# Optimization experiments

Measured on AMD Instinct MI355X. Metric: run time of the kernel, lower is better.

Reference implementation:

```python
import jax, jax.numpy as jnp
import numpy as np

N, F, H, C = 50000, 128, 256, 40
E = 800000
L, J = 3, 2
TOT = 7  # sum_{i<L} J**i


def setup_inputs() -> dict:
    key = jax.random.key(0)
    ks = jax.random.split(key, 16)
    def rn(k, shape, scale):
        return jax.random.normal(k, shape, jnp.float32) * scale
    w = lambda k, shape: rn(k, shape, 1.0 / np.sqrt(shape[0]).astype(np.float32))
    return {
        "x": rn(ks[0], (N, F), 1.0),
        "feature": rn(ks[1], (TOT, N, F), 1.0),
        "src": jax.random.randint(ks[2], (E,), 0, N),
        "dst": jax.random.randint(ks[3], (E,), 0, N),
        "conv_W0": w(ks[4], (F, H)),       "conv_b0": jnp.zeros((H,), jnp.float32),
        "conv_W1": w(ks[5], (2 * H, H)),   "conv_b1": jnp.zeros((H,), jnp.float32),
        "conv_W2": w(ks[6], (2 * H, H)),   "conv_b2": jnp.zeros((H,), jnp.float32),
        "lin_W0": w(ks[7], (F, H)),        "lin_b0": jnp.zeros((H,), jnp.float32),
        "lin_W1": w(ks[8], (2 * F, H)),    "lin_b1": jnp.zeros((H,), jnp.float32),
        "lin_W2": w(ks[9], (4 * F, H)),    "lin_b2": jnp.zeros((H,), jnp.float32),
        "order_weights": rn(ks[10], (J,), 1.0 / np.sqrt(J).astype(np.float32)),
        "cls_W": w(ks[11], (2 * H, C)),    "cls_b": jnp.zeros((C,), jnp.float32),
    }


def reference(x, feature, src, dst,
              conv_W0, conv_b0, conv_W1, conv_b1, conv_W2, conv_b2,
              lin_W0, lin_b0, lin_W1, lin_b1, lin_W2, lin_b2,
              order_weights, cls_W, cls_b):
    # GCN normalization with self-loops (A-hat = D^-1/2 (A+I) D^-1/2)
    loop = jnp.arange(N, dtype=src.dtype)
    src_sl = jnp.concatenate([src, loop])   # [E+N]
    dst_sl = jnp.concatenate([dst, loop])
    deg = jax.ops.segment_sum(jnp.ones_like(dst_sl, jnp.float32), dst_sl, num_segments=N)
    dinv = jax.lax.rsqrt(deg)  # deg >= 1 thanks to self loops
    norm = dinv[src_sl] * dinv[dst_sl]      # [E+N]

    def gcn(h, W, b):
        m = h @ W                            # transform first (smaller gather)
        agg = jax.ops.segment_sum(m[src_sl] * norm[:, None], dst_sl, num_segments=N)
        return agg + b

    conv_W = [conv_W0, conv_W1, conv_W2]
    conv_b = [conv_b0, conv_b1, conv_b2]
    lin_W = [lin_W0, lin_W1, lin_W2]
    lin_b = [lin_b0, lin_b1, lin_b2]

    comb = x
    begin = 0
    for i in range(L):
        convx = jax.nn.relu(gcn(comb, conv_W[i], conv_b[i]))  # [N, H]
        count = J ** i
        lf = feature[begin:begin + count]                      # [count, N, F]
        if i > 0:
            ow = jnp.tile(order_weights, J ** (i - 1)).reshape(-1, 1, 1)
            lf = ow * lf
        lf = jnp.moveaxis(lf, 0, 1).reshape(N, count * F)      # [N, count*F]
        lin_sct = jax.nn.relu(lf @ lin_W[i] + lin_b[i])        # [N, H]
        comb = jnp.concatenate([lin_sct, convx], axis=-1)      # [N, 2H]
        begin += count
    logits = gcn(comb, cls_W, cls_b)                           # [N, C]
    return jax.nn.log_softmax(logits, axis=-1), logits
```

## Files before the change

### kernel.cpp

```cpp
#include <hip/hip_runtime.h>

#define DEVI __device__ __forceinline__

namespace {

constexpr int Nn = 50000;
constexpr int Ne = 800000;
constexpr int Fd = 128;
constexpr int Hd = 256;
constexpr int Cd = 40;
constexpr int NB = (Nn + 255) / 256;

typedef __attribute__((ext_vector_type(8))) short s16x8;
typedef __attribute__((ext_vector_type(8))) unsigned short u16x8;
typedef __attribute__((ext_vector_type(4))) float f32x4;

DEVI unsigned short f2bf(float f) {
  unsigned int u = __builtin_bit_cast(unsigned int, f);
  u += 0x7fffu + ((u >> 16) & 1u);
  return (unsigned short)(u >> 16);
}
DEVI float bf2f(unsigned short s) {
  return __builtin_bit_cast(float, ((unsigned int)s) << 16);
}

DEVI void gld_lds16(const void* gptr, void* lds_base) {
  const unsigned m0v =
      (unsigned)__builtin_amdgcn_readfirstlane((unsigned)(uintptr_t)lds_base);
  asm volatile("s_mov_b32 m0, %0\n\t"
               "global_load_lds_dwordx4 %1, off"
               :: "s"(m0v), "v"(gptr) : "memory");
}

DEVI void wt_one(const float* __restrict__ W, unsigned short* __restrict__ Wt,
                 int idx, int K, int H) {
  int c = idx / K, k = idx - c * K;
  int kt = k >> 6, c16 = (k >> 3) & 7, j = k & 7;
  int ksrc = (kt << 6) | ((c16 ^ (c & 7)) << 3) | j;
  float v = (c < H) ? W[(size_t)ksrc * H + c] : 0.0f;
  Wt[idx] = f2bf(v);
}

constexpr int WTO0 = 0;
constexpr int WTO1 = WTO0 + 256 * 128;
constexpr int WTO2 = WTO1 + 256 * 512;
constexpr int WTO3 = WTO2 + 256 * 512;
constexpr int WTO4 = WTO3 + 256 * 128;
constexpr int WTO5 = WTO4 + 256 * 256;
constexpr int WTO6 = WTO5 + 256 * 512;
constexpr int WTO7 = WTO6 + 64 * 512;
constexpr int PREPTOT = WTO7 + Nn;

__global__ __launch_bounds__(256) void k_prep(
    const float* W0, const float* W1, const float* W2, const float* W3,
    const float* W4, const float* W5, const float* W6,
    unsigned short* T0, unsigned short* T1, unsigned short* T2, unsigned short* T3,
    unsigned short* T4, unsigned short* T5, unsigned short* T6, int* cnt) {
  int idx = blockIdx.x * 256 + threadIdx.x;
  if (idx >= PREPTOT) return;
  if (idx < WTO1)      wt_one(W0, T0, idx - WTO0, 128, 256);
  else if (idx < WTO2) wt_one(W1, T1, idx - WTO1, 512, 256);
  else if (idx < WTO3) wt_one(W2, T2, idx - WTO2, 512, 256);
  else if (idx < WTO4) wt_one(W3, T3, idx - WTO3, 128, 256);
  else if (idx < WTO5) wt_one(W4, T4, idx - WTO4, 256, 256);
  else if (idx < WTO6) wt_one(W5, T5, idx - WTO5, 512, 256);
  else if (idx < WTO7) wt_one(W6, T6, idx - WTO6, 512, 40);
  else cnt[idx - WTO7] = 0;
}

__global__ void k_count(const int* __restrict__ dst, int* __restrict__ cnt) {
  int e = blockIdx.x * 256 + threadIdx.x;
  if (e < Ne) atomicAdd(&cnt[dst[e]], 1);
}

__global__ __launch_bounds__(256) void k_partial(const int* __restrict__ cnt,
                                                 int* __restrict__ partial) {
  __shared__ int red[256];
  const int t = threadIdx.x;
  const int i = blockIdx.x * 256 + t;
  red[t] = (i < Nn) ? cnt[i] + 1 : 0;
  __syncthreads();
#pragma unroll
  for (int off = 128; off; off >>= 1) {
    if (t < off) red[t] += red[t + off];
    __syncthreads();
  }
  if (t == 0) partial[blockIdx.x] = red[0];
}

__global__ __launch_bounds__(256) void k_scan_small(const int* __restrict__ partial,
                                                    int* __restrict__ poffs,
                                                    int* __restrict__ rowptr) {
  __shared__ int s[256];
  const int t = threadIdx.x;
  const int v = (t < NB) ? partial[t] : 0;
  s[t] = v;
  __syncthreads();
#pragma unroll
  for (int off = 1; off < 256; off <<= 1) {
    int add = (t >= off) ? s[t - off] : 0;
    __syncthreads();
    s[t] += add;
    __syncthreads();
  }
  if (t < NB) poffs[t] = s[t] - v;
  if (t == NB - 1) rowptr[Nn] = s[t];
}

__global__ __launch_bounds__(256) void k_rowptr(const int* __restrict__ cnt,
                                                const int* __restrict__ poffs,
                                                int* __restrict__ rowptr,
                                                int* __restrict__ cursor,
                                                float* __restrict__ dinv) {
  __shared__ int s[256];
  const int t = threadIdx.x;
  const int i = blockIdx.x * 256 + t;
  const int c = (i < Nn) ? cnt[i] + 1 : 0;
  s[t] = c;
  __syncthreads();
#pragma unroll
  for (int off = 1; off < 256; off <<= 1) {
    int add = (t >= off) ? s[t - off] : 0;
    __syncthreads();
    s[t] += add;
    __syncthreads();
  }
  if (i < Nn) {
    const int excl = s[t] - c + poffs[blockIdx.x];
    rowptr[i] = excl;
    cursor[i] = excl;
    dinv[i] = rsqrtf((float)c);
  }
}

__global__ void k_fill(const int* __restrict__ src, const int* __restrict__ dst,
                       const float* __restrict__ dinv, int* __restrict__ cursor,
                       int* __restrict__ csrs, float* __restrict__ csrn) {
  int e = blockIdx.x * 256 + threadIdx.x;
  if (e < Ne) {
    int s = src[e], d = dst[e];
    int pos = atomicAdd(&cursor[d], 1);
    csrs[pos] = s;
    csrn[pos] = dinv[s] * dinv[d];
  } else if (e < Ne + Nn) {
    int d = e - Ne;
    int pos = atomicAdd(&cursor[d], 1);
    csrs[pos] = d;
    float v = dinv[d];
    csrn[pos] = v * v;
  }
}

struct GRole {
  const float* A;
  const unsigned short* Wt;
  const float* ow;
  const float* bias;
  unsigned short* C;
  int K;
  int ldc;
  int relu;
};

__global__ __launch_bounds__(256) void k_gemm4(GRole R0, GRole R1, GRole R2, GRole R3) {
  const GRole R = (blockIdx.y == 0) ? R0 : (blockIdx.y == 1) ? R1
                  : (blockIdx.y == 2) ? R2 : R3;
  __shared__ short lA[2][64 * 64];
  __shared__ short lB[2][256 * 64];
  const int tid = threadIdx.x;
  const int lane = tid & 63;
  const int wid = tid >> 6;
  const int wc = wid;
  const int row0 = blockIdx.x * 64;
  const size_t NnF = (size_t)Nn * Fd;

  f32x4 acc[4][4];
#pragma unroll
  for (int i = 0; i < 4; ++i)
#pragma unroll
    for (int j = 0; j < 4; ++j) acc[i][j] = (f32x4)0.0f;

  auto issueA = [&](int kt, f32x4 (&A4)[2][2]) {
    const int k0 = kt * 64;
    const int c = k0 >> 7;
    const int f0 = k0 & 127;
#pragma unroll
    for (int i = 0; i < 2; ++i) {
      const int v = tid * 2 + i;
      const int row = v >> 3, c16 = v & 7;
      const int grow = row0 + row;
      const bool rv = grow < Nn;
      const float* p = R.A + (size_t)c * NnF + (size_t)grow * Fd + f0 + c16 * 8;
      A4[i][0] = rv ? *(const f32x4*)p : (f32x4)0.0f;
      A4[i][1] = rv ? *(const f32x4*)(p + 4) : (f32x4)0.0f;
    }
  };
  auto writeA = [&](int kt, f32x4 (&A4)[2][2], short* lAb) {
    const float scale = R.ow ? R.ow[(kt >> 1) & 1] : 1.0f;
#pragma unroll
    for (int i = 0; i < 2; ++i) {
      const int v = tid * 2 + i;
      const int row = v >> 3, c16 = v & 7;
      s16x8 val;
#pragma unroll
      for (int q = 0; q < 4; ++q) val[q] = (short)f2bf(A4[i][0][q] * scale);
#pragma unroll
      for (int q = 0; q < 4; ++q) val[4 + q] = (short)f2bf(A4[i][1][q] * scale);
      int byte = row * 128 + c16 * 16;
      byte ^= (row & 7) << 4;
      *(s16x8*)((char*)lAb + byte) = val;
    }
  };
  auto issueB = [&](int kt, short* lBb) {
    const int k0 = kt * 64;
#pragma unroll
    for (int i = 0; i < 8; ++i) {
      const int iss = wid * 8 + i;
      const int col = iss * 8 + (lane >> 3);
      gld_lds16(R.Wt + (size_t)col * R.K + k0 + (lane & 7) * 8, lBb + iss * 512);
    }
  };
  auto compute = [&](const short* lAb, const short* lBb) {
#pragma unroll
    for (int kk = 0; kk < 2; ++kk) {
      s16x8 af[4], bv[4];
#pragma unroll
      for (int mi = 0; mi < 4; ++mi) {
        int r = mi * 16 + (lane & 15);
        int byte = r * 128 + kk * 64 + (lane >> 4) * 16;
        byte ^= (r & 7) << 4;
        af[mi] = *(const s16x8*)((const char*)lAb + byte);
      }
#pragma unroll
      for (int ni = 0; ni < 4; ++ni) {
        int c = wc * 64 + ni * 16 + (lane & 15);
        int byte = c * 128 + kk * 64 + (lane >> 4) * 16;
        byte ^= (c & 7) << 4;
        bv[ni] = *(const s16x8*)((const char*)lBb + byte);
      }
#pragma unroll
      for (int mi = 0; mi < 4; ++mi)
#pragma unroll
        for (int ni = 0; ni < 4; ++ni)
          acc[mi][ni] = __builtin_amdgcn_mfma_f32_16x16x32_bf16(af[mi], bv[ni], acc[mi][ni], 0, 0, 0);
    }
  };

  const int nkt = R.K >> 6;
  f32x4 Areg[2][2];
  issueA(0, Areg);
  issueB(0, lB[0]);
  asm volatile("s_waitcnt vmcnt(0)" ::: "memory");
  writeA(0, Areg, lA[0]);
  __syncthreads();
  int cur = 0;
  for (int kt = 0; kt < nkt - 1; ++kt) {
    f32x4 Anext[2][2];
    issueA(kt + 1, Anext);
    issueB(kt + 1, lB[cur ^ 1]);
    compute(lA[cur], lB[cur]);
    asm volatile("s_waitcnt vmcnt(0)" ::: "memory");
    writeA(kt + 1, Anext, lA[cur ^ 1]);
    __syncthreads();
    cur ^= 1;
  }
  compute(lA[cur], lB[cur]);

#pragma unroll
  for (int ni = 0; ni < 4; ++ni) {
    const int col = wc * 64 + ni * 16 + (lane & 15);
    const float bvl = R.bias ? R.bias[col] : 0.0f;
#pragma unroll
    for (int mi = 0; mi < 4; ++mi) {
      const int rb = row0 + mi * 16 + ((lane >> 4) << 2);
#pragma unroll
      for (int q = 0; q < 4; ++q) {
        int r = rb + q;
        if (r < Nn) {
          float vv = acc[mi][ni][q] + bvl;
          if (R.relu) vv = fmaxf(vv, 0.0f);
          R.C[(size_t)r * R.ldc + col] = f2bf(vv);
        }
      }
    }
  }
}

template <int NWC>
__global__ __launch_bounds__(256) void k_gemmB(
    const unsigned short* __restrict__ A, int lda, int K,
    const unsigned short* __restrict__ Wt, unsigned short* __restrict__ C,
    int ldc, int ncols) {
  constexpr int WRN = 4 / NWC;
  constexpr int BM = WRN * 64;
  constexpr int BN = NWC * 64;
  constexpr int AISSW = BM / 32;
  constexpr int BISSW = BN / 32;
  __shared__ short lA[2][BM * 64];
  __shared__ short lB[2][BN * 64];
  const int tid = threadIdx.x;
  const int lane = tid & 63;
  const int wid = tid >> 6;
  const int wr = wid / NWC;
  const int wc = wid % NWC;
  const int row0 = blockIdx.x * BM;
  const int c16a = (lane & 7) ^ ((lane >> 3) & 7);

  f32x4 acc[4][4];
#pragma unroll
  for (int i = 0; i < 4; ++i)
#pragma unroll
    for (int j = 0; j < 4; ++j) acc[i][j] = (f32x4)0.0f;

  auto stage = [&](int kt, short* lAb, short* lBb) {
    const int k0 = kt * 64;
#pragma unroll
    for (int i = 0; i < AISSW; ++i) {
      const int iss = wid * AISSW + i;
      const int row = row0 + iss * 8 + (lane >> 3);
      gld_lds16(A + (size_t)row * lda + k0 + c16a * 8, lAb + iss * 512);
    }
#pragma unroll
    for (int i = 0; i < BISSW; ++i) {
      const int iss = wid * BISSW + i;
      const int col = iss * 8 + (lane >> 3);
      gld_lds16(Wt + (size_t)col * K + k0 + (lane & 7) * 8, lBb + iss * 512);
    }
  };
  auto compute = [&](const short* lAb, const short* lBb) {
#pragma unroll
    for (int kk = 0; kk < 2; ++kk) {
      s16x8 af[4], bv[4];
#pragma unroll
      for (int mi = 0; mi < 4; ++mi) {
        int r = wr * 64 + mi * 16 + (lane & 15);
        int byte = r * 128 + kk * 64 + (lane >> 4) * 16;
        byte ^= (r & 7) << 4;
        af[mi] = *(const s16x8*)((const char*)lAb + byte);
      }
#pragma unroll
      for (int ni = 0; ni < 4; ++ni) {
        int c = wc * 64 + ni * 16 + (lane & 15);
        int byte = c * 128 + kk * 64 + (lane >> 4) * 16;
        byte ^= (c & 7) << 4;
        bv[ni] = *(const s16x8*)((const char*)lBb + byte);
      }
#pragma unroll
      for (int mi = 0; mi < 4; ++mi)
#pragma unroll
        for (int ni = 0; ni < 4; ++ni)
          acc[mi][ni] = __builtin_amdgcn_mfma_f32_16x16x32_bf16(af[mi], bv[ni], acc[mi][ni], 0, 0, 0);
    }
  };

  const int nkt = K >> 6;
  stage(0, lA[0], lB[0]);
  asm volatile("s_waitcnt vmcnt(0)" ::: "memory");
  __syncthreads();
  int cur = 0;
  for (int kt = 0; kt < nkt - 1; ++kt) {
    stage(kt + 1, lA[cur ^ 1], lB[cur ^ 1]);
    compute(lA[cur], lB[cur]);
    asm volatile("s_waitcnt vmcnt(0)" ::: "memory");
    __syncthreads();
    cur ^= 1;
  }
  compute(lA[cur], lB[cur]);

#pragma unroll
  for (int ni = 0; ni < 4; ++ni) {
    const int col = wc * 64 + ni * 16 + (lane & 15);
    if (col >= ncols) continue;
#pragma unroll
    for (int mi = 0; mi < 4; ++mi) {
      const int rb = row0 + wr * 64 + mi * 16 + ((lane >> 4) << 2);
#pragma unroll
      for (int q = 0; q < 4; ++q) {
        int r = rb + q;
        if (r < Nn) C[(size_t)r * ldc + col] = f2bf(acc[mi][ni][q]);
      }
    }
  }
}

__global__ __launch_bounds__(256) void k_gather(
    const unsigned short* __restrict__ m, const int* __restrict__ rowptr,
    const int* __restrict__ csrs, const float* __restrict__ csrn,
    const float* __restrict__ bias, unsigned short* __restrict__ outp,
    int ldc, int col_off) {
  const int wid = (blockIdx.x * 256 + threadIdx.x) >> 6;
  const int lane = threadIdx.x & 63;
  if (wid >= Nn) return;
  const int half = lane >> 5;
  const int sub = lane & 31;
  const int e0 = rowptr[wid], e1 = rowptr[wid + 1];
  const unsigned short* mcol = m + sub * 8;
  float acc[8];
#pragma unroll
  for (int q = 0; q < 8; ++q) acc[q] = 0.f;

  for (int base = e0; base < e1; base += 64) {
    const int idx = base + lane;
    int s_ = 0;
    float w_ = 0.f;
    if (idx < e1) { s_ = csrs[idx]; w_ = csrn[idx]; }
    const int cn = min(64, e1 - base);
    const int npair = (cn + 1) >> 1;
    float w0, w1, w2, w3;
    u16x8 v0, v1, v2, v3;
    auto pick = [&](int p, float& w, u16x8& v) {
      if (p < npair) {
        const int j = 2 * p + half;
        const int ss = __shfl(s_, j);
        w = __shfl(w_, j);
        v = *(const u16x8*)(mcol + (size_t)ss * Hd);
      } else { w = 0.f; v = (u16x8)0; }
    };
    pick(0, w0, v0); pick(1, w1, v1); pick(2, w2, v2); pick(3, w3, v3);
    for (int p0 = 0; p0 < npair; p0 += 4) {
#pragma unroll
      for (int q = 0; q < 8; ++q) acc[q] += w0 * bf2f(v0[q]);
      pick(p0 + 4, w0, v0);
#pragma unroll
      for (int q = 0; q < 8; ++q) acc[q] += w1 * bf2f(v1[q]);
      pick(p0 + 5, w1, v1);
#pragma unroll
      for (int q = 0; q < 8; ++q) acc[q] += w2 * bf2f(v2[q]);
      pick(p0 + 6, w2, v2);
#pragma unroll
      for (int q = 0; q < 8; ++q) acc[q] += w3 * bf2f(v3[q]);
      pick(p0 + 7, w3, v3);
    }
  }

#pragma unroll
  for (int q = 0; q < 8; ++q) acc[q] += __shfl_xor(acc[q], 32);
  if (half == 0) {
    u16x8 o;
#pragma unroll
    for (int q = 0; q < 8; ++q) {
      float v = fmaxf(acc[q] + bias[sub * 8 + q], 0.f);
      o[q] = f2bf(v);
    }
    *(u16x8*)(outp + (size_t)wid * ldc + col_off + sub * 8) = o;
  }
}

__global__ __launch_bounds__(256) void k_gcls(
    const unsigned short* __restrict__ mc, const int* __restrict__ rowptr,
    const int* __restrict__ csrs, const float* __restrict__ csrn,
    const float* __restrict__ clsb, float* __restrict__ outp) {
  const int wid = (blockIdx.x * 256 + threadIdx.x) >> 6;
  const int lane = threadIdx.x & 63;
  if (wid >= Nn) return;
  const int half = lane >> 5;
  const int sub = lane & 31;
  const bool act = sub < 5;
  const int e0 = rowptr[wid], e1 = rowptr[wid + 1];
  float acc[8];
#pragma unroll
  for (int q = 0; q < 8; ++q) acc[q] = 0.f;

  for (int base = e0; base < e1; base += 64) {
    const int idx = base + lane;
    int s_ = 0;
    float w_ = 0.f;
    if (idx < e1) { s_ = csrs[idx]; w_ = csrn[idx]; }
    const int cn = min(64, e1 - base);
    const int npair = (cn + 1) >> 1;
    int sA = __shfl(s_, half);
    float wA = __shfl(w_, half);
    u16x8 vA = act ? *(const u16x8*)(mc + (size_t)sA * Cd + sub * 8) : (u16x8)0;
    for (int jj = 1; jj < npair; ++jj) {
      const int j = 2 * jj + half;
      const int sB = __shfl(s_, j);
      const float wB = __shfl(w_, j);
      const u16x8 vB = act ? *(const u16x8*)(mc + (size_t)sB * Cd + sub * 8) : (u16x8)0;
#pragma unroll
      for (int q = 0; q < 8; ++q) acc[q] += wA * bf2f(vA[q]);
      wA = wB; vA = vB;
    }
#pragma unroll
    for (int q = 0; q < 8; ++q) acc[q] += wA * bf2f(vA[q]);
  }

#pragma unroll
  for (int q = 0; q < 8; ++q) acc[q] += __shfl_xor(acc[q], 32);

  float l[8];
  float mx = -3.4e38f;
  if (act) {
#pragma unroll
    for (int q = 0; q < 8; ++q) {
      l[q] = acc[q] + clsb[sub * 8 + q];
      mx = fmaxf(mx, l[q]);
    }
  }
#pragma unroll
  for (int off = 1; off < 8; off <<= 1) mx = fmaxf(mx, __shfl_xor(mx, off));
  float se = 0.f;
  if (act) {
#pragma unroll
    for (int q = 0; q < 8; ++q) se += expf(l[q] - mx);
  }
#pragma unroll
  for (int off = 1; off < 8; off <<= 1) se += __shfl_xor(se, off);
  const float lse = mx + logf(se);
  if (half == 0 && act) {
    float* o1 = outp + (size_t)wid * Cd + sub * 8;
    float* o2 = o1 + (size_t)Nn * Cd;
#pragma unroll
    for (int q = 0; q < 8; ++q) {
      o1[q] = l[q] - lse;
      o2[q] = l[q];
    }
  }
}

}

extern "C" void kernel_launch(void* const* d_in, const int* in_sizes, int n_in,
                              void* d_out, int out_size, void* d_ws, size_t ws_size,
                              hipStream_t stream) {
  (void)in_sizes; (void)n_in; (void)out_size; (void)ws_size;
  const float* x       = (const float*)d_in[0];
  const float* feature = (const float*)d_in[1];
  const int* src       = (const int*)d_in[2];
  const int* dst       = (const int*)d_in[3];
  const float* convW[3] = {(const float*)d_in[4], (const float*)d_in[6], (const float*)d_in[8]};
  const float* convB[3] = {(const float*)d_in[5], (const float*)d_in[7], (const float*)d_in[9]};
  const float* linW[3]  = {(const float*)d_in[10], (const float*)d_in[12], (const float*)d_in[14]};
  const float* linB[3]  = {(const float*)d_in[11], (const float*)d_in[13], (const float*)d_in[15]};
  const float* oweights = (const float*)d_in[16];
  const float* clsW     = (const float*)d_in[17];
  const float* clsB     = (const float*)d_in[18];
  float* out = (float*)d_out;

  char* wsp = (char*)d_ws;
  auto alloc = [&](size_t bytes) -> void* {
    void* p = wsp;
    wsp += (bytes + 255) & ~(size_t)255;
    return p;
  };
  int* cnt      = (int*)alloc((size_t)Nn * 4);
  int* cursor   = (int*)alloc((size_t)Nn * 4);
  int* rowptr   = (int*)alloc((size_t)(Nn + 1) * 4);
  float* dinv   = (float*)alloc((size_t)Nn * 4);
  int* partial  = (int*)alloc((size_t)NB * 4);
  int* poffs    = (int*)alloc((size_t)NB * 4);
  int* csrs     = (int*)alloc((size_t)(Ne + Nn) * 4);
  float* csrn   = (float*)alloc((size_t)(Ne + Nn) * 4);
  unsigned short* WtC0 = (unsigned short*)alloc((size_t)256 * 128 * 2);
  unsigned short* WtC1 = (unsigned short*)alloc((size_t)256 * 512 * 2);
  unsigned short* WtC2 = (unsigned short*)alloc((size_t)256 * 512 * 2);
  unsigned short* WtL0 = (unsigned short*)alloc((size_t)256 * 128 * 2);
  unsigned short* WtL1 = (unsigned short*)alloc((size_t)256 * 256 * 2);
  unsigned short* WtL2 = (unsigned short*)alloc((size_t)256 * 512 * 2);
  unsigned short* WtCl = (unsigned short*)alloc((size_t)64 * 512 * 2);
  unsigned short* mbuf = (unsigned short*)alloc((size_t)Nn * Hd * 2);
  unsigned short* mcls = (unsigned short*)alloc((size_t)Nn * Cd * 2);
  unsigned short* comb0 = (unsigned short*)alloc((size_t)(Nn + 256) * 512 * 2);
  unsigned short* comb1 = (unsigned short*)alloc((size_t)(Nn + 256) * 512 * 2);
  unsigned short* comb2 = (unsigned short*)alloc((size_t)(Nn + 256) * 512 * 2);

  k_prep<<<(PREPTOT + 255) / 256, 256, 0, stream>>>(
      convW[0], convW[1], convW[2], linW[0], linW[1], linW[2], clsW,
      WtC0, WtC1, WtC2, WtL0, WtL1, WtL2, WtCl, cnt);
  k_count<<<(Ne + 255) / 256, 256, 0, stream>>>(dst, cnt);
  k_partial<<<NB, 256, 0, stream>>>(cnt, partial);
  k_scan_small<<<1, 256, 0, stream>>>(partial, poffs, rowptr);
  k_rowptr<<<NB, 256, 0, stream>>>(cnt, poffs, rowptr, cursor, dinv);
  k_fill<<<(Ne + Nn + 255) / 256, 256, 0, stream>>>(src, dst, dinv, cursor, csrs, csrn);

  const int GM = (Nn + 63) / 64;
  const int GC = (Nn + 255) / 256;
  const int GB = (Nn * 64) / 256;

  GRole rConv0{x,                              WtC0, nullptr,  nullptr, mbuf,  128, Hd,  0};
  GRole rLin0 {feature,                        WtL0, nullptr,  linB[0], comb0, 128, 512, 1};
  GRole rLin1 {feature + (size_t)1 * Nn * Fd,  WtL1, oweights, linB[1], comb1, 256, 512, 1};
  GRole rLin2 {feature + (size_t)3 * Nn * Fd,  WtL2, oweights, linB[2], comb2, 512, 512, 1};
  k_gemm4<<<dim3(GM, 4), 256, 0, stream>>>(rConv0, rLin0, rLin1, rLin2);

  k_gather<<<GB, 256, 0, stream>>>(mbuf, rowptr, csrs, csrn, convB[0], comb0, 512, 256);
  k_gemmB<4><<<GM, 256, 0, stream>>>(comb0, 512, 512, WtC1, mbuf, Hd, 256);
  k_gather<<<GB, 256, 0, stream>>>(mbuf, rowptr, csrs, csrn, convB[1], comb1, 512, 256);
  k_gemmB<4><<<GM, 256, 0, stream>>>(comb1, 512, 512, WtC2, mbuf, Hd, 256);
  k_gather<<<GB, 256, 0, stream>>>(mbuf, rowptr, csrs, csrn, convB[2], comb2, 512, 256);
  k_gemmB<1><<<GC, 256, 0, stream>>>(comb2, 512, 512, WtCl, mcls, Cd, 40);
  k_gcls<<<GB, 256, 0, stream>>>(mcls, rowptr, csrs, csrn, clsB, out);
}
```

Before: 537.6 us.

## Load GEMM weight fragments directly from global, drop LDS B staging, fold order weights

The GEMM kernels no longer stage the weight (B) tiles through LDS. Each wave now reads its bf16 weight fragments straight from global memory (expected to hit L2) into registers, which removes the swizzled LDS layout of the transposed weights and shrinks shared memory use. The order weights are folded into the lin1/lin2 weights during prep instead of scaling activations in the GEMM. This should save LDS traffic and raise occupancy, but weight loads now sit on the compute critical path with no prefetch and may be less coalesced.

New measurement: 585.1 us. 1.09x slower.

```diff
diff --git a/kernel.cpp b/kernel.cpp
--- a/kernel.cpp
+++ b/kernel.cpp
@@ -33,11 +33,10 @@
 }
 
 DEVI void wt_one(const float* __restrict__ W, unsigned short* __restrict__ Wt,
-                 int idx, int K, int H) {
+                 int idx, int K, int H, const float* __restrict__ ow) {
   int c = idx / K, k = idx - c * K;
-  int kt = k >> 6, c16 = (k >> 3) & 7, j = k & 7;
-  int ksrc = (kt << 6) | ((c16 ^ (c & 7)) << 3) | j;
-  float v = (c < H) ? W[(size_t)ksrc * H + c] : 0.0f;
+  float v = (c < H) ? W[(size_t)k * H + c] : 0.0f;
+  if (ow) v *= ow[(k >> 7) & 1];
   Wt[idx] = f2bf(v);
 }
 
@@ -53,18 +52,18 @@
 
 __global__ __launch_bounds__(256) void k_prep(
     const float* W0, const float* W1, const float* W2, const float* W3,
-    const float* W4, const float* W5, const float* W6,
+    const float* W4, const float* W5, const float* W6, const float* ow,
     unsigned short* T0, unsigned short* T1, unsigned short* T2, unsigned short* T3,
     unsigned short* T4, unsigned short* T5, unsigned short* T6, int* cnt) {
   int idx = blockIdx.x * 256 + threadIdx.x;
   if (idx >= PREPTOT) return;
-  if (idx < WTO1)      wt_one(W0, T0, idx - WTO0, 128, 256);
-  else if (idx < WTO2) wt_one(W1, T1, idx - WTO1, 512, 256);
-  else if (idx < WTO3) wt_one(W2, T2, idx - WTO2, 512, 256);
-  else if (idx < WTO4) wt_one(W3, T3, idx - WTO3, 128, 256);
-  else if (idx < WTO5) wt_one(W4, T4, idx - WTO4, 256, 256);
-  else if (idx < WTO6) wt_one(W5, T5, idx - WTO5, 512, 256);
-  else if (idx < WTO7) wt_one(W6, T6, idx - WTO6, 512, 40);
+  if (idx < WTO1)      wt_one(W0, T0, idx - WTO0, 128, 256, nullptr);
+  else if (idx < WTO2) wt_one(W1, T1, idx - WTO1, 512, 256, nullptr);
+  else if (idx < WTO3) wt_one(W2, T2, idx - WTO2, 512, 256, nullptr);
+  else if (idx < WTO4) wt_one(W3, T3, idx - WTO3, 128, 256, nullptr);
+  else if (idx < WTO5) wt_one(W4, T4, idx - WTO4, 256, 256, ow);
+  else if (idx < WTO6) wt_one(W5, T5, idx - WTO5, 512, 256, ow);
+  else if (idx < WTO7) wt_one(W6, T6, idx - WTO6, 512, 40, nullptr);
   else cnt[idx - WTO7] = 0;
 }
 
@@ -151,10 +150,20 @@
   }
 }
 
+DEVI void loadB_frags(const unsigned short* __restrict__ Wt, int K, int k0,
+                      int colbase, int lane, s16x8 (&bv)[2][4]) {
+#pragma unroll
+  for (int kk = 0; kk < 2; ++kk)
+#pragma unroll
+    for (int ni = 0; ni < 4; ++ni) {
+      const int col = colbase + ni * 16 + (lane & 15);
+      bv[kk][ni] = *(const s16x8*)(Wt + (size_t)col * K + k0 + kk * 32 + (lane >> 4) * 8);
+    }
+}
+
 struct GRole {
   const float* A;
   const unsigned short* Wt;
-  const float* ow;
   const float* bias;
   unsigned short* C;
   int K;
@@ -166,7 +175,6 @@
   const GRole R = (blockIdx.y == 0) ? R0 : (blockIdx.y == 1) ? R1
                   : (blockIdx.y == 2) ? R2 : R3;
   __shared__ short lA[2][64 * 64];
-  __shared__ short lB[2][256 * 64];
   const int tid = threadIdx.x;
   const int lane = tid & 63;
   const int wid = tid >> 6;
@@ -180,7 +188,7 @@
 #pragma unroll
     for (int j = 0; j < 4; ++j) acc[i][j] = (f32x4)0.0f;
 
-  auto issueA = [&](int kt, f32x4 (&A4)[2][2]) {
+  auto loadA = [&](int kt, f32x4 (&A4)[2][2]) {
     const int k0 = kt * 64;
     const int c = k0 >> 7;
     const int f0 = k0 & 127;
@@ -195,35 +203,27 @@
       A4[i][1] = rv ? *(const f32x4*)(p + 4) : (f32x4)0.0f;
     }
   };
-  auto writeA = [&](int kt, f32x4 (&A4)[2][2], short* lAb) {
-    const float scale = R.ow ? R.ow[(kt >> 1) & 1] : 1.0f;
+  auto writeA = [&](f32x4 (&A4)[2][2], short* lAb) {
 #pragma unroll
     for (int i = 0; i < 2; ++i) {
       const int v = tid * 2 + i;
       const int row = v >> 3, c16 = v & 7;
       s16x8 val;
 #pragma unroll
-      for (int q = 0; q < 4; ++q) val[q] = (short)f2bf(A4[i][0][q] * scale);
-#pragma unroll
-      for (int q = 0; q < 4; ++q) val[4 + q] = (short)f2bf(A4[i][1][q] * scale);
+      for (int q = 0; q < 4; ++q) val[q] = (short)f2bf(A4[i][0][q]);
+#pragma unroll
+      for (int q = 0; q < 4; ++q) val[4 + q] = (short)f2bf(A4[i][1][q]);
       int byte = row * 128 + c16 * 16;
       byte ^= (row & 7) << 4;
       *(s16x8*)((char*)lAb + byte) = val;
     }
   };
-  auto issueB = [&](int kt, short* lBb) {
-    const int k0 = kt * 64;
-#pragma unroll
-    for (int i = 0; i < 8; ++i) {
-      const int iss = wid * 8 + i;
-      const int col = iss * 8 + (lane >> 3);
-      gld_lds16(R.Wt + (size_t)col * R.K + k0 + (lane & 7) * 8, lBb + iss * 512);
-    }
-  };
-  auto compute = [&](const short* lAb, const short* lBb) {
+  auto compute = [&](const short* lAb, int kt) {
+    s16x8 bv[2][4];
+    loadB_frags(R.Wt, R.K, kt * 64, wc * 64, lane, bv);
 #pragma unroll
     for (int kk = 0; kk < 2; ++kk) {
-      s16x8 af[4], bv[4];
+      s16x8 af[4];
 #pragma unroll
       for (int mi = 0; mi < 4; ++mi) {
         int r = mi * 16 + (lane & 15);
@@ -232,39 +232,22 @@
         af[mi] = *(const s16x8*)((const char*)lAb + byte);
       }
 #pragma unroll
-      for (int ni = 0; ni < 4; ++ni) {
-        int c = wc * 64 + ni * 16 + (lane & 15);
-        int byte = c * 128 + kk * 64 + (lane >> 4) * 16;
-        byte ^= (c & 7) << 4;
-        bv[ni] = *(const s16x8*)((const char*)lBb + byte);
-      }
-#pragma unroll
       for (int mi = 0; mi < 4; ++mi)
 #pragma unroll
         for (int ni = 0; ni < 4; ++ni)
-          acc[mi][ni] = __builtin_amdgcn_mfma_f32_16x16x32_bf16(af[mi], bv[ni], acc[mi][ni], 0, 0, 0);
+          acc[mi][ni] = __builtin_amdgcn_mfma_f32_16x16x32_bf16(af[mi], bv[kk][ni], acc[mi][ni], 0, 0, 0);
     }
   };
 
   const int nkt = R.K >> 6;
   f32x4 Areg[2][2];
-  issueA(0, Areg);
-  issueB(0, lB[0]);
-  asm volatile("s_waitcnt vmcnt(0)" ::: "memory");
-  writeA(0, Areg, lA[0]);
-  __syncthreads();
-  int cur = 0;
-  for (int kt = 0; kt < nkt - 1; ++kt) {
-    f32x4 Anext[2][2];
-    issueA(kt + 1, Anext);
-    issueB(kt + 1, lB[cur ^ 1]);
-    compute(lA[cur], lB[cur]);
-    asm volatile("s_waitcnt vmcnt(0)" ::: "memory");
-    writeA(kt + 1, Anext, lA[cur ^ 1]);
-    __syncthreads();
-    cur ^= 1;
-  }
-  compute(lA[cur], lB[cur]);
+  loadA(0, Areg);
+  for (int kt = 0; kt < nkt; ++kt) {
+    writeA(Areg, lA[kt & 1]);
+    if (kt + 1 < nkt) loadA(kt + 1, Areg);
+    __syncthreads();
+    compute(lA[kt & 1], kt);
+  }
 
 #pragma unroll
   for (int ni = 0; ni < 4; ++ni) {
@@ -286,18 +269,14 @@
   }
 }
 
-template <int NWC>
+template <int WRN, int NWC>
 __global__ __launch_bounds__(256) void k_gemmB(
     const unsigned short* __restrict__ A, int lda, int K,
     const unsigned short* __restrict__ Wt, unsigned short* __restrict__ C,
     int ldc, int ncols) {
-  constexpr int WRN = 4 / NWC;
   constexpr int BM = WRN * 64;
-  constexpr int BN = NWC * 64;
   constexpr int AISSW = BM / 32;
-  constexpr int BISSW = BN / 32;
   __shared__ short lA[2][BM * 64];
-  __shared__ short lB[2][BN * 64];
   const int tid = threadIdx.x;
   const int lane = tid & 63;
   const int wid = tid >> 6;
@@ -312,7 +291,7 @@
 #pragma unroll
     for (int j = 0; j < 4; ++j) acc[i][j] = (f32x4)0.0f;
 
-  auto stage = [&](int kt, short* lAb, short* lBb) {
+  auto stageA = [&](int kt, short* lAb) {
     const int k0 = kt * 64;
 #pragma unroll
     for (int i = 0; i < AISSW; ++i) {
@@ -320,17 +299,13 @@
       const int row = row0 + iss * 8 + (lane >> 3);
       gld_lds16(A + (size_t)row * lda + k0 + c16a * 8, lAb + iss * 512);
     }
-#pragma unroll
-    for (int i = 0; i < BISSW; ++i) {
-      const int iss = wid * BISSW + i;
-      const int col = iss * 8 + (lane >> 3);
-      gld_lds16(Wt + (size_t)col * K + k0 + (lane & 7) * 8, lBb + iss * 512);
-    }
   };
-  auto compute = [&](const short* lAb, const short* lBb) {
+  auto compute = [&](const short* lAb, int kt) {
+    s16x8 bv[2][4];
+    loadB_frags(Wt, K, kt * 64, wc * 64, lane, bv);
 #pragma unroll
     for (int kk = 0; kk < 2; ++kk) {
-      s16x8 af[4], bv[4];
+      s16x8 af[4];
 #pragma unroll
       for (int mi = 0; mi < 4; ++mi) {
         int r = wr * 64 + mi * 16 + (lane & 15);
@@ -339,33 +314,23 @@
         af[mi] = *(const s16x8*)((const char*)lAb + byte);
       }
 #pragma unroll
-      for (int ni = 0; ni < 4; ++ni) {
-        int c = wc * 64 + ni * 16 + (lane & 15);
-        int byte = c * 128 + kk * 64 + (lane >> 4) * 16;
-        byte ^= (c & 7) << 4;
-        bv[ni] = *(const s16x8*)((const char*)lBb + byte);
-      }
-#pragma unroll
       for (int mi = 0; mi < 4; ++mi)
 #pragma unroll
         for (int ni = 0; ni < 4; ++ni)
-          acc[mi][ni] = __builtin_amdgcn_mfma_f32_16x16x32_bf16(af[mi], bv[ni], acc[mi][ni], 0, 0, 0);
+          acc[mi][ni] = __builtin_amdgcn_mfma_f32_16x16x32_bf16(af[mi], bv[kk][ni], acc[mi][ni], 0, 0, 0);
     }
   };
 
   const int nkt = K >> 6;
-  stage(0, lA[0], lB[0]);
+  stageA(0, lA[0]);
   asm volatile("s_waitcnt vmcnt(0)" ::: "memory");
   __syncthreads();
-  int cur = 0;
-  for (int kt = 0; kt < nkt - 1; ++kt) {
-    stage(kt + 1, lA[cur ^ 1], lB[cur ^ 1]);
-    compute(lA[cur], lB[cur]);
+  for (int kt = 0; kt < nkt; ++kt) {
+    if (kt + 1 < nkt) stageA(kt + 1, lA[(kt + 1) & 1]);
+    compute(lA[kt & 1], kt);
     asm volatile("s_waitcnt vmcnt(0)" ::: "memory");
     __syncthreads();
-    cur ^= 1;
-  }
-  compute(lA[cur], lB[cur]);
+  }
 
 #pragma unroll
   for (int ni = 0; ni < 4; ++ni) {
@@ -564,7 +529,7 @@
   unsigned short* comb2 = (unsigned short*)alloc((size_t)(Nn + 256) * 512 * 2);
 
   k_prep<<<(PREPTOT + 255) / 256, 256, 0, stream>>>(
-      convW[0], convW[1], convW[2], linW[0], linW[1], linW[2], clsW,
+      convW[0], convW[1], convW[2], linW[0], linW[1], linW[2], clsW, oweights,
       WtC0, WtC1, WtC2, WtL0, WtL1, WtL2, WtCl, cnt);
   k_count<<<(Ne + 255) / 256, 256, 0, stream>>>(dst, cnt);
   k_partial<<<NB, 256, 0, stream>>>(cnt, partial);
@@ -576,17 +541,17 @@
   const int GC = (Nn + 255) / 256;
   const int GB = (Nn * 64) / 256;
 
-  GRole rConv0{x,                              WtC0, nullptr,  nullptr, mbuf,  128, Hd,  0};
-  GRole rLin0 {feature,                        WtL0, nullptr,  linB[0], comb0, 128, 512, 1};
-  GRole rLin1 {feature + (size_t)1 * Nn * Fd,  WtL1, oweights, linB[1], comb1, 256, 512, 1};
-  GRole rLin2 {feature + (size_t)3 * Nn * Fd,  WtL2, oweights, linB[2], comb2, 512, 512, 1};
+  GRole rConv0{x,                              WtC0, nullptr, mbuf,  128, Hd,  0};
+  GRole rLin0 {feature,                        WtL0, linB[0], comb0, 128, 512, 1};
+  GRole rLin1 {feature + (size_t)1 * Nn * Fd,  WtL1, linB[1], comb1, 256, 512, 1};
+  GRole rLin2 {feature + (size_t)3 * Nn * Fd,  WtL2, linB[2], comb2, 512, 512, 1};
   k_gemm4<<<dim3(GM, 4), 256, 0, stream>>>(rConv0, rLin0, rLin1, rLin2);
 
   k_gather<<<GB, 256, 0, stream>>>(mbuf, rowptr, csrs, csrn, convB[0], comb0, 512, 256);
-  k_gemmB<4><<<GM, 256, 0, stream>>>(comb0, 512, 512, WtC1, mbuf, Hd, 256);
+  k_gemmB<1, 4><<<GM, 256, 0, stream>>>(comb0, 512, 512, WtC1, mbuf, Hd, 256);
   k_gather<<<GB, 256, 0, stream>>>(mbuf, rowptr, csrs, csrn, convB[1], comb1, 512, 256);
-  k_gemmB<4><<<GM, 256, 0, stream>>>(comb1, 512, 512, WtC2, mbuf, Hd, 256);
+  k_gemmB<1, 4><<<GM, 256, 0, stream>>>(comb1, 512, 512, WtC2, mbuf, Hd, 256);
   k_gather<<<GB, 256, 0, stream>>>(mbuf, rowptr, csrs, csrn, convB[2], comb2, 512, 256);
-  k_gemmB<1><<<GC, 256, 0, stream>>>(comb2, 512, 512, WtCl, mcls, Cd, 40);
+  k_gemmB<4, 1><<<GC, 256, 0, stream>>>(comb2, 512, 512, WtCl, mcls, Cd, 40);
   k_gcls<<<GB, 256, 0, stream>>>(mcls, rowptr, csrs, csrn, clsB, out);
 }
```
